# Kernel tuning notes

Measured on AMD Instinct MI355X. Metric: run time of the kernel, lower is better.

The kernel has to match this reference:

```python
import jax, jax.numpy as jnp
import numpy as np

B, L, E, H = 128, 256, 256, 512


def setup_inputs() -> dict:
    key = jax.random.key(0)
    ks = jax.random.split(key, 16)
    s = 0.02
    return {
        "embedded_inputs": jax.random.normal(ks[0], (B, L, E), jnp.float32),
        "decoder_input": jax.random.normal(ks[1], (B, E), jnp.float32),
        "dec_h": jax.random.normal(ks[2], (B, H), jnp.float32),
        "dec_c": jax.random.normal(ks[3], (B, H), jnp.float32),
        "context": jax.random.normal(ks[4], (B, L, H), jnp.float32),
        # Decoder params
        "W_i2h": jax.random.normal(ks[5], (4 * H, E), jnp.float32) * s,
        "b_i2h": jnp.zeros((4 * H,), jnp.float32),
        "W_h2h": jax.random.normal(ks[6], (4 * H, H), jnp.float32) * s,
        "b_h2h": jnp.zeros((4 * H,), jnp.float32),
        "W_out": jax.random.normal(ks[7], (H, 2 * H), jnp.float32) * s,
        "b_out": jnp.zeros((H,), jnp.float32),
        # Attention params
        "W_inp": jax.random.normal(ks[8], (H, H), jnp.float32) * s,
        "b_inp": jnp.zeros((H,), jnp.float32),
        "W_ctx": jax.random.normal(ks[9], (H, H), jnp.float32) * s,  # Conv1d(k=1) kernel squeezed
        "b_ctx": jnp.zeros((H,), jnp.float32),
        "V": jax.random.uniform(ks[10], (H,), jnp.float32, -1.0, 1.0),
    }


def reference(embedded_inputs, decoder_input, dec_h, dec_c, context,
              W_i2h, b_i2h, W_h2h, b_h2h, W_out, b_out,
              W_inp, b_inp, W_ctx, b_ctx, V):
    # Precompute projected context: Conv1d(k=1) == per-position linear. ctx: [B, H, L]
    ctx = jnp.einsum("blh,gh->bgl", context, W_ctx) + b_ctx[None, :, None]
    seq_len = embedded_inputs.shape[1]

    def step(carry, _):
        x, h, c, mask = carry
        gates = x @ W_i2h.T + b_i2h + h @ W_h2h.T + b_h2h
        i, f, g, o = jnp.split(gates, 4, axis=1)
        c_t = jax.nn.sigmoid(f) * c + jax.nn.sigmoid(i) * jnp.tanh(g)
        h_t = jax.nn.sigmoid(o) * jnp.tanh(c_t)
        # attention
        inp = h_t @ W_inp.T + b_inp                              # [B, H]
        scores = jnp.einsum("h,bhl->bl", V, jnp.tanh(inp[:, :, None] + ctx))
        att = jnp.where(mask == 0, -jnp.inf, scores)
        alpha = jax.nn.softmax(att, axis=-1)                     # [B, L]
        hidden = jnp.einsum("bhl,bl->bh", ctx, alpha)
        h_new = jnp.tanh(jnp.concatenate([hidden, h_t], axis=1) @ W_out.T + b_out)
        # pointer selection
        idx = jnp.argmax(alpha * mask, axis=1)                   # [B]
        one_hot = jax.nn.one_hot(idx, seq_len, dtype=mask.dtype)
        mask_new = mask * (1.0 - one_hot)
        next_x = jnp.take_along_axis(embedded_inputs, idx[:, None, None], axis=1)[:, 0, :]
        return (next_x, h_new, c_t, mask_new), (alpha, idx)

    mask0 = jnp.ones((embedded_inputs.shape[0], seq_len), jnp.float32)
    (x_f, h_f, c_f, _), (alphas, ptrs) = jax.lax.scan(
        step, (decoder_input, dec_h, dec_c, mask0), None, length=seq_len)
    outputs = jnp.transpose(alphas, (1, 0, 2))   # [B, L, L]
    pointers = jnp.transpose(ptrs, (1, 0))       # [B, L]
    return outputs, pointers, h_f, c_f
```

## Files before the change

### kernel.cpp

```cpp
#include <hip/hip_runtime.h>

#define B 128
#define L 256
#define E 256
#define H 512
#define NBLK 256
#define NTHR 512

typedef float f4 __attribute__((ext_vector_type(4)));

#define WS_CTX 0u
#define WS_HT  18874368u
#define WS_HH  18939904u
#define WS_HID 19005440u
#define WS_INP 19071232u
#define WS_XT  19136768u
#define WS_FLG 19169536u

#define OUT_ALPHA 0u
#define OUT_PTR   8388608u
#define OUT_H     8421376u
#define OUT_C     8486912u

#define L2E 1.4426950408889634f

__device__ __forceinline__ float fast_rcp(float x) { return __builtin_amdgcn_rcpf(x); }

__device__ __forceinline__ float ftanh(float x) {
  float e = exp2f(x * (2.0f * L2E));
  return 1.0f - 2.0f * fast_rcp(e + 1.0f);
}
__device__ __forceinline__ float fsig(float x) {
  float e = exp2f(-x * L2E);
  return fast_rcp(1.0f + e);
}

#define CLD1(v0, p0)                                                          \
  asm volatile("global_load_dwordx4 %0, %1, off sc0 sc1\n\t"                  \
               "s_waitcnt vmcnt(0)"                                           \
               : "=&v"(v0) : "v"(p0) : "memory")

#define CLD2(va, pa)                                                          \
  asm volatile("global_load_dwordx4 %0, %2, off sc0 sc1\n\t"                  \
               "global_load_dwordx4 %1, %3, off sc0 sc1\n\t"                  \
               "s_waitcnt vmcnt(0)"                                           \
               : "=&v"(va[0]), "=&v"(va[1])                                   \
               : "v"(pa[0]), "v"(pa[1]) : "memory")

#define CLD4(va, pa)                                                          \
  asm volatile("global_load_dwordx4 %0, %4, off sc0 sc1\n\t"                  \
               "global_load_dwordx4 %1, %5, off sc0 sc1\n\t"                  \
               "global_load_dwordx4 %2, %6, off sc0 sc1\n\t"                  \
               "global_load_dwordx4 %3, %7, off sc0 sc1\n\t"                  \
               "s_waitcnt vmcnt(0)"                                           \
               : "=&v"(va[0]), "=&v"(va[1]), "=&v"(va[2]), "=&v"(va[3])       \
               : "v"(pa[0]), "v"(pa[1]), "v"(pa[2]), "v"(pa[3]) : "memory")

#define CLD6(va, pa)                                                          \
  asm volatile("global_load_dwordx4 %0, %6, off sc0 sc1\n\t"                  \
               "global_load_dwordx4 %1, %7, off sc0 sc1\n\t"                  \
               "global_load_dwordx4 %2, %8, off sc0 sc1\n\t"                  \
               "global_load_dwordx4 %3, %9, off sc0 sc1\n\t"                  \
               "global_load_dwordx4 %4, %10, off sc0 sc1\n\t"                 \
               "global_load_dwordx4 %5, %11, off sc0 sc1\n\t"                 \
               "s_waitcnt vmcnt(0)"                                           \
               : "=&v"(va[0]), "=&v"(va[1]), "=&v"(va[2]), "=&v"(va[3]),      \
                 "=&v"(va[4]), "=&v"(va[5])                                   \
               : "v"(pa[0]), "v"(pa[1]), "v"(pa[2]), "v"(pa[3]),              \
                 "v"(pa[4]), "v"(pa[5]) : "memory")

#define CST4_1(p0, v0)                                                        \
  asm volatile("global_store_dwordx4 %0, %1, off sc0 sc1\n\t"                 \
               "s_waitcnt expcnt(0)"                                          \
               :: "v"(p0), "v"(v0) : "memory")

__device__ __forceinline__ void gbar(unsigned* flags, unsigned tgt) {
  asm volatile("s_waitcnt vmcnt(0) lgkmcnt(0) expcnt(0)" ::: "memory");
  __syncthreads();
  if (threadIdx.x == 0) {
    unsigned* p = flags + blockIdx.x * 16;
    asm volatile("global_store_dword %0, %1, off sc0 sc1" :: "v"(p), "v"(tgt) : "memory");
  }
  if (blockIdx.x == 0) {
    if (threadIdx.x < 64) {
      const unsigned* p0 = flags + (threadIdx.x * 4 + 0) * 16;
      const unsigned* p1 = flags + (threadIdx.x * 4 + 1) * 16;
      const unsigned* p2 = flags + (threadIdx.x * 4 + 2) * 16;
      const unsigned* p3 = flags + (threadIdx.x * 4 + 3) * 16;
      for (;;) {
        unsigned f0, f1, f2, f3;
        asm volatile("global_load_dword %0, %4, off sc0 sc1\n\t"
                     "global_load_dword %1, %5, off sc0 sc1\n\t"
                     "global_load_dword %2, %6, off sc0 sc1\n\t"
                     "global_load_dword %3, %7, off sc0 sc1\n\t"
                     "s_waitcnt vmcnt(0)"
                     : "=&v"(f0), "=&v"(f1), "=&v"(f2), "=&v"(f3)
                     : "v"(p0), "v"(p1), "v"(p2), "v"(p3) : "memory");
        if (__all(f0 >= tgt && f1 >= tgt && f2 >= tgt && f3 >= tgt)) break;
        __builtin_amdgcn_s_sleep(1);
      }
    }
    __syncthreads();
    if (threadIdx.x < 8) {
      unsigned* gp = flags + 4096 + threadIdx.x * 16;
      asm volatile("global_store_dword %0, %1, off sc0 sc1" :: "v"(gp), "v"(tgt) : "memory");
    }
  } else {
    if (threadIdx.x == 0) {
      const unsigned* gp = flags + 4096 + (blockIdx.x & 7) * 16;
      for (;;) {
        unsigned g;
        asm volatile("global_load_dword %0, %1, off sc0 sc1\n\ts_waitcnt vmcnt(0)"
                     : "=&v"(g) : "v"(gp) : "memory");
        if (g >= tgt) break;
        __builtin_amdgcn_s_sleep(2);
      }
    }
  }
  __syncthreads();
}

__global__ __launch_bounds__(256) void k_ctx(const float* __restrict__ context,
                                             const float* __restrict__ Wc,
                                             const float* __restrict__ bc,
                                             float* __restrict__ ws) {
  __shared__ float a_lds[64][33];
  __shared__ float b_lds[32][68];
  int t = threadIdx.x;
  int m0 = blockIdx.x * 64;
  int n0 = blockIdx.y * 64;
  int tx = t & 15, ty = t >> 4;
  float acc[4][4] = {};
  for (int kc = 0; kc < 16; ++kc) {
    int k0 = kc * 32;
    __syncthreads();
#pragma unroll
    for (int i = 0; i < 2; ++i) {
      int f40 = t + i * 256;
      int mm = f40 >> 3;
      int k4 = (f40 & 7) * 4;
      float4 v = *(const float4*)&context[(size_t)(m0 + mm) * H + k0 + k4];
      a_lds[mm][k4] = v.x; a_lds[mm][k4 + 1] = v.y; a_lds[mm][k4 + 2] = v.z; a_lds[mm][k4 + 3] = v.w;
    }
#pragma unroll
    for (int i = 0; i < 2; ++i) {
      int f40 = t + i * 256;
      int nn = f40 >> 3;
      int k4 = (f40 & 7) * 4;
      float4 v = *(const float4*)&Wc[(size_t)(n0 + nn) * H + k0 + k4];
      b_lds[k4][nn] = v.x; b_lds[k4 + 1][nn] = v.y; b_lds[k4 + 2][nn] = v.z; b_lds[k4 + 3][nn] = v.w;
    }
    __syncthreads();
#pragma unroll
    for (int kk = 0; kk < 32; ++kk) {
      float4 bv = *(const float4*)&b_lds[kk][tx * 4];
      float a0 = a_lds[ty * 4 + 0][kk], a1 = a_lds[ty * 4 + 1][kk];
      float a2 = a_lds[ty * 4 + 2][kk], a3 = a_lds[ty * 4 + 3][kk];
      acc[0][0] += a0 * bv.x; acc[0][1] += a0 * bv.y; acc[0][2] += a0 * bv.z; acc[0][3] += a0 * bv.w;
      acc[1][0] += a1 * bv.x; acc[1][1] += a1 * bv.y; acc[1][2] += a1 * bv.z; acc[1][3] += a1 * bv.w;
      acc[2][0] += a2 * bv.x; acc[2][1] += a2 * bv.y; acc[2][2] += a2 * bv.z; acc[2][3] += a2 * bv.w;
      acc[3][0] += a3 * bv.x; acc[3][1] += a3 * bv.y; acc[3][2] += a3 * bv.z; acc[3][3] += a3 * bv.w;
    }
  }
  float b0v = bc[n0 + tx * 4], b1v = bc[n0 + tx * 4 + 1], b2v = bc[n0 + tx * 4 + 2], b3v = bc[n0 + tx * 4 + 3];
#pragma unroll
  for (int i = 0; i < 4; ++i) {
    size_t o = WS_CTX + (size_t)(m0 + ty * 4 + i) * H + n0 + tx * 4;
    float4 v; v.x = acc[i][0] + b0v; v.y = acc[i][1] + b1v; v.z = acc[i][2] + b2v; v.w = acc[i][3] + b3v;
    *(float4*)&ws[o] = v;
  }
}

__global__ __launch_bounds__(256) void k_init(const float* __restrict__ dec_h,
                                              const float* __restrict__ dec_in,
                                              float* __restrict__ ws) {
  int flat = blockIdx.x * 256 + threadIdx.x;
  if (flat < 65536) {
    ws[WS_HH + flat] = dec_h[flat];
  } else if (flat < 98304) {
    ws[WS_XT + (flat - 65536)] = dec_in[flat - 65536];
  } else if (flat < 102528) {
    ((unsigned*)(ws + WS_FLG))[flat - 98304] = 0u;
  }
}

__global__ __launch_bounds__(512, 1) void k_main(
    const float* __restrict__ Wi2h, const float* __restrict__ bi2h,
    const float* __restrict__ Wh2h, const float* __restrict__ bh2h,
    const float* __restrict__ Wout, const float* __restrict__ bout,
    const float* __restrict__ Winp, const float* __restrict__ binp,
    const float* __restrict__ Vv,   const float* __restrict__ emb,
    const float* __restrict__ dec_c,
    float* __restrict__ ws,         float* __restrict__ out) {
  __shared__ float s_act[13504];
  __shared__ float s_maskP[256];
  __shared__ float s_mw[8], s_dw[8];
  __shared__ float s_red[4];
  __shared__ int   s_redi[4];
  __shared__ int   s_wc[4], s_wb[4];
  __shared__ int   s_mi, s_cnt;

  unsigned* flags = (unsigned*)(ws + WS_FLG);
  const int bid = blockIdx.x;
  const int t = threadIdx.x;
  const int wv = t >> 6, ln = t & 63;
  unsigned tgt = 0;

  float creg = 0.f;

  if (bid < 128 && t < 256) s_maskP[t] = 1.0f;
  __syncthreads();

  for (int step = 0; step < L; ++step) {
    {
      const int jt = (bid & 7) * 4 + ((bid >> 3) & 3);
      const int bt = bid >> 5;
      const int u0 = jt * 16, b0 = bt * 16;
      float* sact = s_act;
      float* sg   = s_act + 12352;
      f4 va[6]; const float* pa[6]; int sb[6], sq[6];
#pragma unroll
      for (int it = 0; it < 6; ++it) {
        unsigned c = (unsigned)(t + it * 512);
        int bl = (int)(c / 192u);
        int kq = (int)(c - (unsigned)bl * 192u);
        int kg = kq * 4;
        sb[it] = bl; sq[it] = kq;
        pa[it] = (kg < 256) ? ws + WS_XT + (size_t)(b0 + bl) * 256 + kg
                            : ws + WS_HH + (size_t)(b0 + bl) * 512 + (kg - 256);
      }
      CLD6(va, pa);
      __builtin_amdgcn_sched_barrier(0);
#pragma unroll
      for (int it = 0; it < 6; ++it) *(f4*)&sact[sb[it] * 772 + sq[it] * 4] = va[it];
      __syncthreads();

      const int jj = t >> 4, bb = t & 15;
      const int g = jj >> 3, up = (jj & 7) * 2;
      const int r0 = g * 512 + u0 + up;
      float a0 = 0.f, a1 = 0.f;
      {
        const float* w0 = Wi2h + (size_t)r0 * 256;
        const float* w1 = w0 + 256;
        const float* sa = sact + bb * 772;
#pragma unroll 8
        for (int k4 = 0; k4 < 64; ++k4) {
          float4 x = *(const float4*)&sa[k4 * 4];
          float4 p = *(const float4*)&w0[k4 * 4];
          float4 q = *(const float4*)&w1[k4 * 4];
          a0 += p.x * x.x + p.y * x.y + p.z * x.z + p.w * x.w;
          a1 += q.x * x.x + q.y * x.y + q.z * x.z + q.w * x.w;
        }
        const float* v0 = Wh2h + (size_t)r0 * 512;
        const float* v1 = v0 + 512;
        const float* shh = sa + 256;
#pragma unroll 8
        for (int k4 = 0; k4 < 128; ++k4) {
          float4 x = *(const float4*)&shh[k4 * 4];
          float4 p = *(const float4*)&v0[k4 * 4];
          float4 q = *(const float4*)&v1[k4 * 4];
          a0 += p.x * x.x + p.y * x.y + p.z * x.z + p.w * x.w;
          a1 += q.x * x.x + q.y * x.y + q.z * x.z + q.w * x.w;
        }
      }
      sg[(g * 16 + up) * 17 + bb]     = a0;
      sg[(g * 16 + up + 1) * 17 + bb] = a1;
      __syncthreads();
      if (t < 256) {
        const int uu = t >> 4, b2 = t & 15;
        const int j0 = u0 + uu;
        float si_ = sg[(     uu) * 17 + b2] + bi2h[       j0] + bh2h[       j0];
        float sf_ = sg[(16 + uu) * 17 + b2] + bi2h[ 512 + j0] + bh2h[ 512 + j0];
        float sg_ = sg[(32 + uu) * 17 + b2] + bi2h[1024 + j0] + bh2h[1024 + j0];
        float so_ = sg[(48 + uu) * 17 + b2] + bi2h[1536 + j0] + bh2h[1536 + j0];
        if (step == 0) creg = dec_c[(size_t)(b0 + b2) * 512 + j0];
        float cn = fsig(sf_) * creg + fsig(si_) * ftanh(sg_);
        creg = cn;
        float htv = fsig(so_) * ftanh(cn);
        s_act[b2 * 17 + uu] = htv;
        if (step == L - 1) out[OUT_C + (size_t)(b0 + b2) * 512 + j0] = cn;
      }
      __syncthreads();
      if (t < 64) {
        const int b2 = t >> 2, q = t & 3;
        f4 hv;
        hv[0] = s_act[b2 * 17 + q * 4 + 0];
        hv[1] = s_act[b2 * 17 + q * 4 + 1];
        hv[2] = s_act[b2 * 17 + q * 4 + 2];
        hv[3] = s_act[b2 * 17 + q * 4 + 3];
        float* hp = ws + WS_HT + (size_t)(b0 + b2) * 512 + u0 + q * 4;
        CST4_1(hp, hv);
      }
    }
    ++tgt; gbar(flags, tgt);

    {
      const int gt = (bid & 7) * 2 + ((bid >> 3) & 1);
      const int bt = bid >> 4;
      const int g0 = gt * 32, b0 = bt * 8;
      float* si = s_act;
      float* stmp = s_act + 4128;
      f4 va[2]; const float* pa[2];
#pragma unroll
      for (int it = 0; it < 2; ++it) {
        int c = t + it * 512;
        int bl = c >> 7, kq = c & 127;
        pa[it] = ws + WS_HT + (size_t)(b0 + bl) * 512 + kq * 4;
      }
      CLD2(va, pa);
      __builtin_amdgcn_sched_barrier(0);
#pragma unroll
      for (int it = 0; it < 2; ++it) {
        int c = t + it * 512;
        int bl = c >> 7, kq = c & 127;
        *(f4*)&si[bl * 516 + kq * 4] = va[it];
      }
      __syncthreads();
      if (t < 256) {
        const int gl = t >> 3, bb = t & 7;
        const float* w = Winp + (size_t)(g0 + gl) * 512;
        const float* sa = si + bb * 516;
        float acc = 0.f;
#pragma unroll 8
        for (int k4 = 0; k4 < 128; ++k4) {
          float4 ww = *(const float4*)&w[k4 * 4];
          float4 xx = *(const float4*)&sa[k4 * 4];
          acc += ww.x * xx.x + ww.y * xx.y + ww.z * xx.z + ww.w * xx.w;
        }
        stmp[bb * 33 + gl] = acc + binp[g0 + gl];
      }
      __syncthreads();
      if (t < 64) {
        const int bb = t >> 3, q = t & 7;
        f4 v;
        v[0] = stmp[bb * 33 + q * 4 + 0];
        v[1] = stmp[bb * 33 + q * 4 + 1];
        v[2] = stmp[bb * 33 + q * 4 + 2];
        v[3] = stmp[bb * 33 + q * 4 + 3];
        float* p = ws + WS_INP + (size_t)(b0 + bb) * 512 + g0 + q * 4;
        CST4_1(p, v);
      }
    }
    ++tgt; gbar(flags, tgt);

    if (bid < 128) {
      const int b = bid;
      float* s_inp  = s_act;
      float* s_sc   = s_act + 512;
      int*   s_li   = (int*)(s_act + 768);
      float* s_hidp = s_act + 1024;
      float* s_out  = s_act + 5120;
      if (t < 128) {
        f4 v;
        const float* p = ws + WS_INP + (size_t)b * 512 + t * 4;
        CLD1(v, p);
        *(f4*)&s_inp[t * 4] = v;
      }
      __syncthreads();
      const int d0 = ln * 8;
      float inp8[8], v8[8];
#pragma unroll
      for (int i = 0; i < 8; ++i) { inp8[i] = s_inp[d0 + i]; v8[i] = Vv[d0 + i]; }
      bool validl = (t < 256) && (s_maskP[t] != 0.f);
      unsigned long long bal = __ballot(validl);
      if (t < 256 && (t & 63) == 0) s_wc[t >> 6] = (int)__popcll(bal);
      __syncthreads();
      if (t == 0) {
        int base = 0;
#pragma unroll
        for (int i = 0; i < 4; ++i) { s_wb[i] = base; base += s_wc[i]; }
        s_cnt = base;
      }
      __syncthreads();
      if (validl) {
        int idx = s_wb[t >> 6] + (int)__popcll(bal & ((1ull << (t & 63)) - 1ull));
        s_li[idx] = t;
      }
      __syncthreads();
      const int cnt = s_cnt;
      float m = -INFINITY, den = 0.f;
      float hid[8] = {0, 0, 0, 0, 0, 0, 0, 0};
      {
        f4 cur0a, cur0b, cur1a, cur1b, cur2a, cur2b, cur3a, cur3b;
        int l0i, l1i, l2i, l3i;
        int base = wv * 4;
        {
          int s0 = base, s1 = base + 1, s2 = base + 2, s3 = base + 3;
          int a = (s0 < cnt) ? s_li[s0] : 0;  l0i = (s0 < cnt) ? a : -1;
          int bb2 = (s1 < cnt) ? s_li[s1] : 0; l1i = (s1 < cnt) ? bb2 : -1;
          int c = (s2 < cnt) ? s_li[s2] : 0;  l2i = (s2 < cnt) ? c : -1;
          int d = (s3 < cnt) ? s_li[s3] : 0;  l3i = (s3 < cnt) ? d : -1;
          const f4* p0 = (const f4*)(ws + WS_CTX + ((size_t)(b * 256 + a) * 512) + d0);
          const f4* p1 = (const f4*)(ws + WS_CTX + ((size_t)(b * 256 + bb2) * 512) + d0);
          const f4* p2 = (const f4*)(ws + WS_CTX + ((size_t)(b * 256 + c) * 512) + d0);
          const f4* p3 = (const f4*)(ws + WS_CTX + ((size_t)(b * 256 + d) * 512) + d0);
          cur0a = __builtin_nontemporal_load(p0); cur0b = __builtin_nontemporal_load(p0 + 1);
          cur1a = __builtin_nontemporal_load(p1); cur1b = __builtin_nontemporal_load(p1 + 1);
          cur2a = __builtin_nontemporal_load(p2); cur2b = __builtin_nontemporal_load(p2 + 1);
          cur3a = __builtin_nontemporal_load(p3); cur3b = __builtin_nontemporal_load(p3 + 1);
        }
        for (; base < cnt; base += 32) {
          f4 n0a, n0b, n1a, n1b, n2a, n2b, n3a, n3b;
          int nl0, nl1, nl2, nl3;
          {
            int s0 = base + 32, s1 = base + 33, s2 = base + 34, s3 = base + 35;
            int a = (s0 < cnt) ? s_li[s0] : 0;  nl0 = (s0 < cnt) ? a : -1;
            int bb2 = (s1 < cnt) ? s_li[s1] : 0; nl1 = (s1 < cnt) ? bb2 : -1;
            int c = (s2 < cnt) ? s_li[s2] : 0;  nl2 = (s2 < cnt) ? c : -1;
            int d = (s3 < cnt) ? s_li[s3] : 0;  nl3 = (s3 < cnt) ? d : -1;
            const f4* p0 = (const f4*)(ws + WS_CTX + ((size_t)(b * 256 + a) * 512) + d0);
            const f4* p1 = (const f4*)(ws + WS_CTX + ((size_t)(b * 256 + bb2) * 512) + d0);
            const f4* p2 = (const f4*)(ws + WS_CTX + ((size_t)(b * 256 + c) * 512) + d0);
            const f4* p3 = (const f4*)(ws + WS_CTX + ((size_t)(b * 256 + d) * 512) + d0);
            n0a = __builtin_nontemporal_load(p0); n0b = __builtin_nontemporal_load(p0 + 1);
            n1a = __builtin_nontemporal_load(p1); n1b = __builtin_nontemporal_load(p1 + 1);
            n2a = __builtin_nontemporal_load(p2); n2b = __builtin_nontemporal_load(p2 + 1);
            n3a = __builtin_nontemporal_load(p3); n3b = __builtin_nontemporal_load(p3 + 1);
          }
          float sv0, sv1, sv2, sv3;
          {
            float part = v8[0] * ftanh(inp8[0] + cur0a[0]) + v8[1] * ftanh(inp8[1] + cur0a[1])
                       + v8[2] * ftanh(inp8[2] + cur0a[2]) + v8[3] * ftanh(inp8[3] + cur0a[3])
                       + v8[4] * ftanh(inp8[4] + cur0b[0]) + v8[5] * ftanh(inp8[5] + cur0b[1])
                       + v8[6] * ftanh(inp8[6] + cur0b[2]) + v8[7] * ftanh(inp8[7] + cur0b[3]);
#pragma unroll
            for (int off = 32; off > 0; off >>= 1) part += __shfl_xor(part, off);
            if (l0i >= 0 && ln == 0) s_sc[l0i] = part;
            sv0 = (l0i >= 0) ? part : -INFINITY;
          }
          {
            float part = v8[0] * ftanh(inp8[0] + cur1a[0]) + v8[1] * ftanh(inp8[1] + cur1a[1])
                       + v8[2] * ftanh(inp8[2] + cur1a[2]) + v8[3] * ftanh(inp8[3] + cur1a[3])
                       + v8[4] * ftanh(inp8[4] + cur1b[0]) + v8[5] * ftanh(inp8[5] + cur1b[1])
                       + v8[6] * ftanh(inp8[6] + cur1b[2]) + v8[7] * ftanh(inp8[7] + cur1b[3]);
#pragma unroll
            for (int off = 32; off > 0; off >>= 1) part += __shfl_xor(part, off);
            if (l1i >= 0 && ln == 0) s_sc[l1i] = part;
            sv1 = (l1i >= 0) ? part : -INFINITY;
          }
          {
            float part = v8[0] * ftanh(inp8[0] + cur2a[0]) + v8[1] * ftanh(inp8[1] + cur2a[1])
                       + v8[2] * ftanh(inp8[2] + cur2a[2]) + v8[3] * ftanh(inp8[3] + cur2a[3])
                       + v8[4] * ftanh(inp8[4] + cur2b[0]) + v8[5] * ftanh(inp8[5] + cur2b[1])
                       + v8[6] * ftanh(inp8[6] + cur2b[2]) + v8[7] * ftanh(inp8[7] + cur2b[3]);
#pragma unroll
            for (int off = 32; off > 0; off >>= 1) part += __shfl_xor(part, off);
            if (l2i >= 0 && ln == 0) s_sc[l2i] = part;
            sv2 = (l2i >= 0) ? part : -INFINITY;
          }
          {
            float part = v8[0] * ftanh(inp8[0] + cur3a[0]) + v8[1] * ftanh(inp8[1] + cur3a[1])
                       + v8[2] * ftanh(inp8[2] + cur3a[2]) + v8[3] * ftanh(inp8[3] + cur3a[3])
                       + v8[4] * ftanh(inp8[4] + cur3b[0]) + v8[5] * ftanh(inp8[5] + cur3b[1])
                       + v8[6] * ftanh(inp8[6] + cur3b[2]) + v8[7] * ftanh(inp8[7] + cur3b[3]);
#pragma unroll
            for (int off = 32; off > 0; off >>= 1) part += __shfl_xor(part, off);
            if (l3i >= 0 && ln == 0) s_sc[l3i] = part;
            sv3 = (l3i >= 0) ? part : -INFINITY;
          }
          float mn = fmaxf(m, fmaxf(fmaxf(sv0, sv1), fmaxf(sv2, sv3)));
          float scale = exp2f((m - mn) * L2E);
          float e0 = exp2f((sv0 - mn) * L2E);
          float e1 = exp2f((sv1 - mn) * L2E);
          float e2 = exp2f((sv2 - mn) * L2E);
          float e3 = exp2f((sv3 - mn) * L2E);
          den = den * scale + ((e0 + e1) + (e2 + e3));
          hid[0] = hid[0] * scale + e0 * cur0a[0] + e1 * cur1a[0] + e2 * cur2a[0] + e3 * cur3a[0];
          hid[1] = hid[1] * scale + e0 * cur0a[1] + e1 * cur1a[1] + e2 * cur2a[1] + e3 * cur3a[1];
          hid[2] = hid[2] * scale + e0 * cur0a[2] + e1 * cur1a[2] + e2 * cur2a[2] + e3 * cur3a[2];
          hid[3] = hid[3] * scale + e0 * cur0a[3] + e1 * cur1a[3] + e2 * cur2a[3] + e3 * cur3a[3];
          hid[4] = hid[4] * scale + e0 * cur0b[0] + e1 * cur1b[0] + e2 * cur2b[0] + e3 * cur3b[0];
          hid[5] = hid[5] * scale + e0 * cur0b[1] + e1 * cur1b[1] + e2 * cur2b[1] + e3 * cur3b[1];
          hid[6] = hid[6] * scale + e0 * cur0b[2] + e1 * cur1b[2] + e2 * cur2b[2] + e3 * cur3b[2];
          hid[7] = hid[7] * scale + e0 * cur0b[3] + e1 * cur1b[3] + e2 * cur2b[3] + e3 * cur3b[3];
          m = mn;
          cur0a = n0a; cur0b = n0b; cur1a = n1a; cur1b = n1b;
          cur2a = n2a; cur2b = n2b; cur3a = n3a; cur3b = n3b;
          l0i = nl0; l1i = nl1; l2i = nl2; l3i = nl3;
        }
      }
      if (ln == 0) { s_mw[wv] = m; s_dw[wv] = den; }
      __syncthreads();
      float M = s_mw[0];
#pragma unroll
      for (int w = 1; w < 8; ++w) M = fmaxf(M, s_mw[w]);
      float D = 0.f;
#pragma unroll
      for (int w = 0; w < 8; ++w) D += s_dw[w] * exp2f((s_mw[w] - M) * L2E);
      float fac = exp2f((m - M) * L2E);
#pragma unroll
      for (int i = 0; i < 8; ++i) s_hidp[wv * 512 + d0 + i] = hid[i] * fac;
      __syncthreads();
      const float rD = 1.0f / D;
      {
        float hs = 0.f;
#pragma unroll
        for (int w = 0; w < 8; ++w) hs += s_hidp[w * 512 + t];
        s_out[t] = hs * rD;
      }
      float sc = 0.f; bool valid = false;
      if (t < 256) {
        valid = (s_maskP[t] != 0.f);
        sc = s_sc[t];
        float alpha = valid ? exp2f((sc - M) * L2E) * rD : 0.f;
        out[OUT_ALPHA + ((size_t)b * 256 + step) * 256 + t] = alpha;
        float bs = valid ? sc : -INFINITY;
        int bi = t;
#pragma unroll
        for (int off = 32; off > 0; off >>= 1) {
          float os = __shfl_down(bs, off);
          int oi = __shfl_down(bi, off);
          if (os > bs || (os == bs && oi < bi)) { bs = os; bi = oi; }
        }
        if ((t & 63) == 0) { s_red[t >> 6] = bs; s_redi[t >> 6] = bi; }
      }
      __syncthreads();
      if (t == 0) {
        float mm = s_red[0]; int mi = s_redi[0];
#pragma unroll
        for (int w = 1; w < 4; ++w) {
          if (s_red[w] > mm || (s_red[w] == mm && s_redi[w] < mi)) { mm = s_red[w]; mi = s_redi[w]; }
        }
        s_mi = mi;
      }
      __syncthreads();
      const int mi = s_mi;
      if (t < 128) {
        f4 hv = *(const f4*)&s_out[t * 4];
        float* hp = ws + WS_HID + (size_t)b * 512 + t * 4;
        CST4_1(hp, hv);
      }
      if (t < 64) {
        float4 xv = *(const float4*)&emb[((size_t)b * 256 + mi) * 256 + t * 4];
        f4 xq; xq[0] = xv.x; xq[1] = xv.y; xq[2] = xv.z; xq[3] = xv.w;
        float* xp = ws + WS_XT + (size_t)b * 256 + t * 4;
        CST4_1(xp, xq);
      }
      if (t == 0) {
        out[OUT_PTR + (size_t)b * 256 + step] = (float)mi;
        s_maskP[mi] = 0.f;
      }
    }
    ++tgt; gbar(flags, tgt);

    {
      const int rt = (bid & 7) * 2 + ((bid >> 3) & 1);
      const int bt = bid >> 4;
      const int r0 = rt * 32, b0 = bt * 8;
      float* sh = s_act;
      float* stmp = s_act + 8224;
      f4 va[4]; const float* pa[4];
#pragma unroll
      for (int it = 0; it < 4; ++it) {
        int c = t + it * 512;
        int bl = c >> 8, kq = c & 255;
        int kg = kq * 4;
        pa[it] = (kg < 512) ? ws + WS_HID + (size_t)(b0 + bl) * 512 + kg
                            : ws + WS_HT + (size_t)(b0 + bl) * 512 + (kg - 512);
      }
      CLD4(va, pa);
      __builtin_amdgcn_sched_barrier(0);
#pragma unroll
      for (int it = 0; it < 4; ++it) {
        int c = t + it * 512;
        int bl = c >> 8, kq = c & 255;
        *(f4*)&sh[bl * 1028 + kq * 4] = va[it];
      }
      __syncthreads();
      if (t < 256) {
        const int rl = t >> 3, bb = t & 7;
        const float* w = Wout + (size_t)(r0 + rl) * 1024;
        const float* sa = sh + bb * 1028;
        float acc = 0.f;
#pragma unroll 8
        for (int k4 = 0; k4 < 256; ++k4) {
          float4 ww = *(const float4*)&w[k4 * 4];
          float4 xx = *(const float4*)&sa[k4 * 4];
          acc += ww.x * xx.x + ww.y * xx.y + ww.z * xx.z + ww.w * xx.w;
        }
        float h = ftanh(acc + bout[r0 + rl]);
        stmp[bb * 33 + rl] = h;
        if (step == L - 1) out[OUT_H + (size_t)(b0 + bb) * 512 + r0 + rl] = h;
      }
      __syncthreads();
      if (t < 64) {
        const int bb = t >> 3, q = t & 7;
        f4 v;
        v[0] = stmp[bb * 33 + q * 4 + 0];
        v[1] = stmp[bb * 33 + q * 4 + 1];
        v[2] = stmp[bb * 33 + q * 4 + 2];
        v[3] = stmp[bb * 33 + q * 4 + 3];
        float* p = ws + WS_HH + (size_t)(b0 + bb) * 512 + r0 + q * 4;
        CST4_1(p, v);
      }
    }
    ++tgt; gbar(flags, tgt);
  }
}

extern "C" void kernel_launch(void* const* d_in, const int* in_sizes, int n_in,
                              void* d_out, int out_size, void* d_ws, size_t ws_size,
                              hipStream_t stream) {
  (void)in_sizes; (void)n_in; (void)out_size; (void)ws_size;
  const float* emb    = (const float*)d_in[0];
  const float* dec_in = (const float*)d_in[1];
  const float* dec_h  = (const float*)d_in[2];
  const float* dec_c  = (const float*)d_in[3];
  const float* ctx_in = (const float*)d_in[4];
  const float* W_i2h  = (const float*)d_in[5];
  const float* b_i2h  = (const float*)d_in[6];
  const float* W_h2h  = (const float*)d_in[7];
  const float* b_h2h  = (const float*)d_in[8];
  const float* W_out  = (const float*)d_in[9];
  const float* b_out  = (const float*)d_in[10];
  const float* W_inp  = (const float*)d_in[11];
  const float* b_inp  = (const float*)d_in[12];
  const float* W_ctx  = (const float*)d_in[13];
  const float* b_ctx  = (const float*)d_in[14];
  const float* Vv     = (const float*)d_in[15];
  float* out = (float*)d_out;
  float* ws  = (float*)d_ws;

  k_ctx<<<dim3(512, 8), 256, 0, stream>>>(ctx_in, W_ctx, b_ctx, ws);
  k_init<<<401, 256, 0, stream>>>(dec_h, dec_in, ws);
  k_main<<<NBLK, NTHR, 0, stream>>>(W_i2h, b_i2h, W_h2h, b_h2h, W_out, b_out,
                                    W_inp, b_inp, Vv, emb, dec_c, ws, out);
}
```

Before: 16.53 ms.

## Replace global barriers with per-producer flag waits and double-buffered state

```diff
diff --git a/kernel.cpp b/kernel.cpp
--- a/kernel.cpp
+++ b/kernel.cpp
@@ -10,12 +10,17 @@
 typedef float f4 __attribute__((ext_vector_type(4)));
 
 #define WS_CTX 0u
-#define WS_HT  18874368u
-#define WS_HH  18939904u
-#define WS_HID 19005440u
-#define WS_INP 19071232u
-#define WS_XT  19136768u
-#define WS_FLG 19169536u
+#define WS_HT  16777216u
+#define WS_HH  16908288u
+#define WS_HID 17039360u
+#define WS_INP 17170432u
+#define WS_XT  17301504u
+#define WS_FLG 17367040u
+
+#define FLG_PG 0u
+#define FLG_PI 4096u
+#define FLG_PA 8192u
+#define FLG_PH 12288u
 
 #define OUT_ALPHA 0u
 #define OUT_PTR   8388608u
@@ -74,51 +79,28 @@
                "s_waitcnt expcnt(0)"                                          \
                :: "v"(p0), "v"(v0) : "memory")
 
-__device__ __forceinline__ void gbar(unsigned* flags, unsigned tgt) {
-  asm volatile("s_waitcnt vmcnt(0) lgkmcnt(0) expcnt(0)" ::: "memory");
-  __syncthreads();
-  if (threadIdx.x == 0) {
-    unsigned* p = flags + blockIdx.x * 16;
-    asm volatile("global_store_dword %0, %1, off sc0 sc1" :: "v"(p), "v"(tgt) : "memory");
+__device__ __forceinline__ void wait_ge(const unsigned* fp, bool act, unsigned tgt) {
+  for (;;) {
+    unsigned f = tgt;
+    if (act) {
+      asm volatile("global_load_dword %0, %1, off sc0 sc1\n\ts_waitcnt vmcnt(0)"
+                   : "=&v"(f) : "v"(fp) : "memory");
+    }
+    if (__all(f >= tgt)) break;
+    __builtin_amdgcn_s_sleep(1);
   }
-  if (blockIdx.x == 0) {
-    if (threadIdx.x < 64) {
-      const unsigned* p0 = flags + (threadIdx.x * 4 + 0) * 16;
-      const unsigned* p1 = flags + (threadIdx.x * 4 + 1) * 16;
-      const unsigned* p2 = flags + (threadIdx.x * 4 + 2) * 16;
-      const unsigned* p3 = flags + (threadIdx.x * 4 + 3) * 16;
-      for (;;) {
-        unsigned f0, f1, f2, f3;
-        asm volatile("global_load_dword %0, %4, off sc0 sc1\n\t"
-                     "global_load_dword %1, %5, off sc0 sc1\n\t"
-                     "global_load_dword %2, %6, off sc0 sc1\n\t"
-                     "global_load_dword %3, %7, off sc0 sc1\n\t"
-                     "s_waitcnt vmcnt(0)"
-                     : "=&v"(f0), "=&v"(f1), "=&v"(f2), "=&v"(f3)
-                     : "v"(p0), "v"(p1), "v"(p2), "v"(p3) : "memory");
-        if (__all(f0 >= tgt && f1 >= tgt && f2 >= tgt && f3 >= tgt)) break;
-        __builtin_amdgcn_s_sleep(1);
-      }
-    }
-    __syncthreads();
-    if (threadIdx.x < 8) {
-      unsigned* gp = flags + 4096 + threadIdx.x * 16;
-      asm volatile("global_store_dword %0, %1, off sc0 sc1" :: "v"(gp), "v"(tgt) : "memory");
-    }
-  } else {
-    if (threadIdx.x == 0) {
-      const unsigned* gp = flags + 4096 + (blockIdx.x & 7) * 16;
-      for (;;) {
-        unsigned g;
-        asm volatile("global_load_dword %0, %1, off sc0 sc1\n\ts_waitcnt vmcnt(0)"
-                     : "=&v"(g) : "v"(gp) : "memory");
-        if (g >= tgt) break;
-        __builtin_amdgcn_s_sleep(2);
-      }
-    }
-  }
-  __syncthreads();
 }
+
+#define PUBLISH(ARROFF) do {                                                  \
+    asm volatile("s_waitcnt vmcnt(0) lgkmcnt(0) expcnt(0)" ::: "memory");     \
+    __syncthreads();                                                          \
+    if (t == 0) {                                                             \
+      unsigned* fp_ = flags + (ARROFF) + (unsigned)bid * 16u;                 \
+      unsigned v_ = (unsigned)(step + 1);                                     \
+      asm volatile("global_store_dword %0, %1, off sc0 sc1"                   \
+                   :: "v"(fp_), "v"(v_) : "memory");                          \
+    }                                                                         \
+  } while (0)
 
 __global__ __launch_bounds__(256) void k_ctx(const float* __restrict__ context,
                                              const float* __restrict__ Wc,
@@ -179,7 +161,7 @@
     ws[WS_HH + flat] = dec_h[flat];
   } else if (flat < 98304) {
     ws[WS_XT + (flat - 65536)] = dec_in[flat - 65536];
-  } else if (flat < 102528) {
+  } else if (flat < 114688) {
     ((unsigned*)(ws + WS_FLG))[flat - 98304] = 0u;
   }
 }
@@ -204,7 +186,6 @@
   const int bid = blockIdx.x;
   const int t = threadIdx.x;
   const int wv = t >> 6, ln = t & 63;
-  unsigned tgt = 0;
 
   float creg = 0.f;
 
@@ -212,10 +193,29 @@
   __syncthreads();
 
   for (int step = 0; step < L; ++step) {
+    const unsigned pr = (unsigned)(step & 1);
+    float* HTc  = ws + WS_HT  + pr * 65536u;
+    float* HHr  = ws + WS_HH  + pr * 65536u;
+    float* HHw  = ws + WS_HH  + (pr ^ 1u) * 65536u;
+    float* HIDc = ws + WS_HID + pr * 65536u;
+    float* INPc = ws + WS_INP + pr * 65536u;
+    float* XTr  = ws + WS_XT  + pr * 32768u;
+    float* XTw  = ws + WS_XT  + (pr ^ 1u) * 32768u;
+
     {
       const int jt = (bid & 7) * 4 + ((bid >> 3) & 3);
       const int bt = bid >> 5;
       const int u0 = jt * 16, b0 = bt * 16;
+      if (step > 0) {
+        if (wv == 0) {
+          const unsigned* fp = flags;
+          bool act = false;
+          if (ln < 32) { fp = flags + FLG_PH + ((unsigned)bt * 32u + (unsigned)ln) * 16u; act = true; }
+          else if (ln < 48) { fp = flags + FLG_PA + ((unsigned)bt * 16u + (unsigned)(ln - 32)) * 16u; act = true; }
+          wait_ge(fp, act, (unsigned)step);
+        }
+        __syncthreads();
+      }
       float* sact = s_act;
       float* sg   = s_act + 12352;
       f4 va[6]; const float* pa[6]; int sb[6], sq[6];
@@ -226,8 +226,8 @@
         int kq = (int)(c - (unsigned)bl * 192u);
         int kg = kq * 4;
         sb[it] = bl; sq[it] = kq;
-        pa[it] = (kg < 256) ? ws + WS_XT + (size_t)(b0 + bl) * 256 + kg
-                            : ws + WS_HH + (size_t)(b0 + bl) * 512 + (kg - 256);
+        pa[it] = (kg < 256) ? XTr + (size_t)(b0 + bl) * 256 + kg
+                            : HHr + (size_t)(b0 + bl) * 512 + (kg - 256);
       }
       CLD6(va, pa);
       __builtin_amdgcn_sched_barrier(0);
@@ -288,16 +288,20 @@
         hv[1] = s_act[b2 * 17 + q * 4 + 1];
         hv[2] = s_act[b2 * 17 + q * 4 + 2];
         hv[3] = s_act[b2 * 17 + q * 4 + 3];
-        float* hp = ws + WS_HT + (size_t)(b0 + b2) * 512 + u0 + q * 4;
+        float* hp = HTc + (size_t)(b0 + b2) * 512 + u0 + q * 4;
         CST4_1(hp, hv);
       }
-    }
-    ++tgt; gbar(flags, tgt);
+      PUBLISH(FLG_PG);
+    }
 
     {
       const int gt = (bid & 7) * 2 + ((bid >> 3) & 1);
       const int bt = bid >> 4;
       const int g0 = gt * 32, b0 = bt * 8;
+      if (wv == 0)
+        wait_ge(flags + FLG_PG + ((unsigned)(bid >> 5) * 32u + (unsigned)ln) * 16u,
+                ln < 32, (unsigned)(step + 1));
+      __syncthreads();
       float* si = s_act;
       float* stmp = s_act + 4128;
       f4 va[2]; const float* pa[2];
@@ -305,7 +309,7 @@
       for (int it = 0; it < 2; ++it) {
         int c = t + it * 512;
         int bl = c >> 7, kq = c & 127;
-        pa[it] = ws + WS_HT + (size_t)(b0 + bl) * 512 + kq * 4;
+        pa[it] = HTc + (size_t)(b0 + bl) * 512 + kq * 4;
       }
       CLD2(va, pa);
       __builtin_amdgcn_sched_barrier(0);
@@ -337,11 +341,11 @@
         v[1] = stmp[bb * 33 + q * 4 + 1];
         v[2] = stmp[bb * 33 + q * 4 + 2];
         v[3] = stmp[bb * 33 + q * 4 + 3];
-        float* p = ws + WS_INP + (size_t)(b0 + bb) * 512 + g0 + q * 4;
+        float* p = INPc + (size_t)(b0 + bb) * 512 + g0 + q * 4;
         CST4_1(p, v);
       }
-    }
-    ++tgt; gbar(flags, tgt);
+      PUBLISH(FLG_PI);
+    }
 
     if (bid < 128) {
       const int b = bid;
@@ -350,17 +354,6 @@
       int*   s_li   = (int*)(s_act + 768);
       float* s_hidp = s_act + 1024;
       float* s_out  = s_act + 5120;
-      if (t < 128) {
-        f4 v;
-        const float* p = ws + WS_INP + (size_t)b * 512 + t * 4;
-        CLD1(v, p);
-        *(f4*)&s_inp[t * 4] = v;
-      }
-      __syncthreads();
-      const int d0 = ln * 8;
-      float inp8[8], v8[8];
-#pragma unroll
-      for (int i = 0; i < 8; ++i) { inp8[i] = s_inp[d0 + i]; v8[i] = Vv[d0 + i]; }
       bool validl = (t < 256) && (s_maskP[t] != 0.f);
       unsigned long long bal = __ballot(validl);
       if (t < 256 && (t & 63) == 0) s_wc[t >> 6] = (int)__popcll(bal);
@@ -378,106 +371,119 @@
       }
       __syncthreads();
       const int cnt = s_cnt;
+      const int d0 = ln * 8;
+      f4 cur0a, cur0b, cur1a, cur1b, cur2a, cur2b, cur3a, cur3b;
+      int l0i, l1i, l2i, l3i;
+      const int base0 = wv * 4;
+      {
+        int s0 = base0, s1 = base0 + 1, s2 = base0 + 2, s3 = base0 + 3;
+        int a = (s0 < cnt) ? s_li[s0] : 0;  l0i = (s0 < cnt) ? a : -1;
+        int bb2 = (s1 < cnt) ? s_li[s1] : 0; l1i = (s1 < cnt) ? bb2 : -1;
+        int c = (s2 < cnt) ? s_li[s2] : 0;  l2i = (s2 < cnt) ? c : -1;
+        int d = (s3 < cnt) ? s_li[s3] : 0;  l3i = (s3 < cnt) ? d : -1;
+        const f4* p0 = (const f4*)(ws + WS_CTX + ((size_t)(b * 256 + a) * 512) + d0);
+        const f4* p1 = (const f4*)(ws + WS_CTX + ((size_t)(b * 256 + bb2) * 512) + d0);
+        const f4* p2 = (const f4*)(ws + WS_CTX + ((size_t)(b * 256 + c) * 512) + d0);
+        const f4* p3 = (const f4*)(ws + WS_CTX + ((size_t)(b * 256 + d) * 512) + d0);
+        cur0a = __builtin_nontemporal_load(p0); cur0b = __builtin_nontemporal_load(p0 + 1);
+        cur1a = __builtin_nontemporal_load(p1); cur1b = __builtin_nontemporal_load(p1 + 1);
+        cur2a = __builtin_nontemporal_load(p2); cur2b = __builtin_nontemporal_load(p2 + 1);
+        cur3a = __builtin_nontemporal_load(p3); cur3b = __builtin_nontemporal_load(p3 + 1);
+      }
+      if (wv == 0)
+        wait_ge(flags + FLG_PI + ((unsigned)(b >> 3) * 16u + (unsigned)ln) * 16u,
+                ln < 16, (unsigned)(step + 1));
+      __syncthreads();
+      if (t < 128) {
+        f4 v;
+        const float* p = INPc + (size_t)b * 512 + t * 4;
+        CLD1(v, p);
+        *(f4*)&s_inp[t * 4] = v;
+      }
+      __syncthreads();
+      float inp8[8], v8[8];
+#pragma unroll
+      for (int i = 0; i < 8; ++i) { inp8[i] = s_inp[d0 + i]; v8[i] = Vv[d0 + i]; }
       float m = -INFINITY, den = 0.f;
       float hid[8] = {0, 0, 0, 0, 0, 0, 0, 0};
-      {
-        f4 cur0a, cur0b, cur1a, cur1b, cur2a, cur2b, cur3a, cur3b;
-        int l0i, l1i, l2i, l3i;
-        int base = wv * 4;
+      for (int base = base0; base < cnt; base += 32) {
+        f4 n0a, n0b, n1a, n1b, n2a, n2b, n3a, n3b;
+        int nl0, nl1, nl2, nl3;
         {
-          int s0 = base, s1 = base + 1, s2 = base + 2, s3 = base + 3;
-          int a = (s0 < cnt) ? s_li[s0] : 0;  l0i = (s0 < cnt) ? a : -1;
-          int bb2 = (s1 < cnt) ? s_li[s1] : 0; l1i = (s1 < cnt) ? bb2 : -1;
-          int c = (s2 < cnt) ? s_li[s2] : 0;  l2i = (s2 < cnt) ? c : -1;
-          int d = (s3 < cnt) ? s_li[s3] : 0;  l3i = (s3 < cnt) ? d : -1;
+          int s0 = base + 32, s1 = base + 33, s2 = base + 34, s3 = base + 35;
+          int a = (s0 < cnt) ? s_li[s0] : 0;  nl0 = (s0 < cnt) ? a : -1;
+          int bb2 = (s1 < cnt) ? s_li[s1] : 0; nl1 = (s1 < cnt) ? bb2 : -1;
+          int c = (s2 < cnt) ? s_li[s2] : 0;  nl2 = (s2 < cnt) ? c : -1;
+          int d = (s3 < cnt) ? s_li[s3] : 0;  nl3 = (s3 < cnt) ? d : -1;
           const f4* p0 = (const f4*)(ws + WS_CTX + ((size_t)(b * 256 + a) * 512) + d0);
           const f4* p1 = (const f4*)(ws + WS_CTX + ((size_t)(b * 256 + bb2) * 512) + d0);
           const f4* p2 = (const f4*)(ws + WS_CTX + ((size_t)(b * 256 + c) * 512) + d0);
           const f4* p3 = (const f4*)(ws + WS_CTX + ((size_t)(b * 256 + d) * 512) + d0);
-          cur0a = __builtin_nontemporal_load(p0); cur0b = __builtin_nontemporal_load(p0 + 1);
-          cur1a = __builtin_nontemporal_load(p1); cur1b = __builtin_nontemporal_load(p1 + 1);
-          cur2a = __builtin_nontemporal_load(p2); cur2b = __builtin_nontemporal_load(p2 + 1);
-          cur3a = __builtin_nontemporal_load(p3); cur3b = __builtin_nontemporal_load(p3 + 1);
-        }
-        for (; base < cnt; base += 32) {
-          f4 n0a, n0b, n1a, n1b, n2a, n2b, n3a, n3b;
-          int nl0, nl1, nl2, nl3;
-          {
-            int s0 = base + 32, s1 = base + 33, s2 = base + 34, s3 = base + 35;
-            int a = (s0 < cnt) ? s_li[s0] : 0;  nl0 = (s0 < cnt) ? a : -1;
-            int bb2 = (s1 < cnt) ? s_li[s1] : 0; nl1 = (s1 < cnt) ? bb2 : -1;
-            int c = (s2 < cnt) ? s_li[s2] : 0;  nl2 = (s2 < cnt) ? c : -1;
-            int d = (s3 < cnt) ? s_li[s3] : 0;  nl3 = (s3 < cnt) ? d : -1;
-            const f4* p0 = (const f4*)(ws + WS_CTX + ((size_t)(b * 256 + a) * 512) + d0);
-            const f4* p1 = (const f4*)(ws + WS_CTX + ((size_t)(b * 256 + bb2) * 512) + d0);
-            const f4* p2 = (const f4*)(ws + WS_CTX + ((size_t)(b * 256 + c) * 512) + d0);
-            const f4* p3 = (const f4*)(ws + WS_CTX + ((size_t)(b * 256 + d) * 512) + d0);
-            n0a = __builtin_nontemporal_load(p0); n0b = __builtin_nontemporal_load(p0 + 1);
-            n1a = __builtin_nontemporal_load(p1); n1b = __builtin_nontemporal_load(p1 + 1);
-            n2a = __builtin_nontemporal_load(p2); n2b = __builtin_nontemporal_load(p2 + 1);
-            n3a = __builtin_nontemporal_load(p3); n3b = __builtin_nontemporal_load(p3 + 1);
-          }
-          float sv0, sv1, sv2, sv3;
-          {
-            float part = v8[0] * ftanh(inp8[0] + cur0a[0]) + v8[1] * ftanh(inp8[1] + cur0a[1])
-                       + v8[2] * ftanh(inp8[2] + cur0a[2]) + v8[3] * ftanh(inp8[3] + cur0a[3])
-                       + v8[4] * ftanh(inp8[4] + cur0b[0]) + v8[5] * ftanh(inp8[5] + cur0b[1])
-                       + v8[6] * ftanh(inp8[6] + cur0b[2]) + v8[7] * ftanh(inp8[7] + cur0b[3]);
-#pragma unroll
-            for (int off = 32; off > 0; off >>= 1) part += __shfl_xor(part, off);
-            if (l0i >= 0 && ln == 0) s_sc[l0i] = part;
-            sv0 = (l0i >= 0) ? part : -INFINITY;
-          }
-          {
-            float part = v8[0] * ftanh(inp8[0] + cur1a[0]) + v8[1] * ftanh(inp8[1] + cur1a[1])
-                       + v8[2] * ftanh(inp8[2] + cur1a[2]) + v8[3] * ftanh(inp8[3] + cur1a[3])
-                       + v8[4] * ftanh(inp8[4] + cur1b[0]) + v8[5] * ftanh(inp8[5] + cur1b[1])
-                       + v8[6] * ftanh(inp8[6] + cur1b[2]) + v8[7] * ftanh(inp8[7] + cur1b[3]);
-#pragma unroll
-            for (int off = 32; off > 0; off >>= 1) part += __shfl_xor(part, off);
-            if (l1i >= 0 && ln == 0) s_sc[l1i] = part;
-            sv1 = (l1i >= 0) ? part : -INFINITY;
-          }
-          {
-            float part = v8[0] * ftanh(inp8[0] + cur2a[0]) + v8[1] * ftanh(inp8[1] + cur2a[1])
-                       + v8[2] * ftanh(inp8[2] + cur2a[2]) + v8[3] * ftanh(inp8[3] + cur2a[3])
-                       + v8[4] * ftanh(inp8[4] + cur2b[0]) + v8[5] * ftanh(inp8[5] + cur2b[1])
-                       + v8[6] * ftanh(inp8[6] + cur2b[2]) + v8[7] * ftanh(inp8[7] + cur2b[3]);
-#pragma unroll
-            for (int off = 32; off > 0; off >>= 1) part += __shfl_xor(part, off);
-            if (l2i >= 0 && ln == 0) s_sc[l2i] = part;
-            sv2 = (l2i >= 0) ? part : -INFINITY;
-          }
-          {
-            float part = v8[0] * ftanh(inp8[0] + cur3a[0]) + v8[1] * ftanh(inp8[1] + cur3a[1])
-                       + v8[2] * ftanh(inp8[2] + cur3a[2]) + v8[3] * ftanh(inp8[3] + cur3a[3])
-                       + v8[4] * ftanh(inp8[4] + cur3b[0]) + v8[5] * ftanh(inp8[5] + cur3b[1])
-                       + v8[6] * ftanh(inp8[6] + cur3b[2]) + v8[7] * ftanh(inp8[7] + cur3b[3]);
-#pragma unroll
-            for (int off = 32; off > 0; off >>= 1) part += __shfl_xor(part, off);
-            if (l3i >= 0 && ln == 0) s_sc[l3i] = part;
-            sv3 = (l3i >= 0) ? part : -INFINITY;
-          }
-          float mn = fmaxf(m, fmaxf(fmaxf(sv0, sv1), fmaxf(sv2, sv3)));
-          float scale = exp2f((m - mn) * L2E);
-          float e0 = exp2f((sv0 - mn) * L2E);
-          float e1 = exp2f((sv1 - mn) * L2E);
-          float e2 = exp2f((sv2 - mn) * L2E);
-          float e3 = exp2f((sv3 - mn) * L2E);
-          den = den * scale + ((e0 + e1) + (e2 + e3));
-          hid[0] = hid[0] * scale + e0 * cur0a[0] + e1 * cur1a[0] + e2 * cur2a[0] + e3 * cur3a[0];
-          hid[1] = hid[1] * scale + e0 * cur0a[1] + e1 * cur1a[1] + e2 * cur2a[1] + e3 * cur3a[1];
-          hid[2] = hid[2] * scale + e0 * cur0a[2] + e1 * cur1a[2] + e2 * cur2a[2] + e3 * cur3a[2];
-          hid[3] = hid[3] * scale + e0 * cur0a[3] + e1 * cur1a[3] + e2 * cur2a[3] + e3 * cur3a[3];
-          hid[4] = hid[4] * scale + e0 * cur0b[0] + e1 * cur1b[0] + e2 * cur2b[0] + e3 * cur3b[0];
-          hid[5] = hid[5] * scale + e0 * cur0b[1] + e1 * cur1b[1] + e2 * cur2b[1] + e3 * cur3b[1];
-          hid[6] = hid[6] * scale + e0 * cur0b[2] + e1 * cur1b[2] + e2 * cur2b[2] + e3 * cur3b[2];
-          hid[7] = hid[7] * scale + e0 * cur0b[3] + e1 * cur1b[3] + e2 * cur2b[3] + e3 * cur3b[3];
-          m = mn;
-          cur0a = n0a; cur0b = n0b; cur1a = n1a; cur1b = n1b;
-          cur2a = n2a; cur2b = n2b; cur3a = n3a; cur3b = n3b;
-          l0i = nl0; l1i = nl1; l2i = nl2; l3i = nl3;
-        }
+          n0a = __builtin_nontemporal_load(p0); n0b = __builtin_nontemporal_load(p0 + 1);
+          n1a = __builtin_nontemporal_load(p1); n1b = __builtin_nontemporal_load(p1 + 1);
+          n2a = __builtin_nontemporal_load(p2); n2b = __builtin_nontemporal_load(p2 + 1);
+          n3a = __builtin_nontemporal_load(p3); n3b = __builtin_nontemporal_load(p3 + 1);
+        }
+        float sv0, sv1, sv2, sv3;
+        {
+          float part = v8[0] * ftanh(inp8[0] + cur0a[0]) + v8[1] * ftanh(inp8[1] + cur0a[1])
+                     + v8[2] * ftanh(inp8[2] + cur0a[2]) + v8[3] * ftanh(inp8[3] + cur0a[3])
+                     + v8[4] * ftanh(inp8[4] + cur0b[0]) + v8[5] * ftanh(inp8[5] + cur0b[1])
+                     + v8[6] * ftanh(inp8[6] + cur0b[2]) + v8[7] * ftanh(inp8[7] + cur0b[3]);
+#pragma unroll
+          for (int off = 32; off > 0; off >>= 1) part += __shfl_xor(part, off);
+          if (l0i >= 0 && ln == 0) s_sc[l0i] = part;
+          sv0 = (l0i >= 0) ? part : -INFINITY;
+        }
+        {
+          float part = v8[0] * ftanh(inp8[0] + cur1a[0]) + v8[1] * ftanh(inp8[1] + cur1a[1])
+                     + v8[2] * ftanh(inp8[2] + cur1a[2]) + v8[3] * ftanh(inp8[3] + cur1a[3])
+                     + v8[4] * ftanh(inp8[4] + cur1b[0]) + v8[5] * ftanh(inp8[5] + cur1b[1])
+                     + v8[6] * ftanh(inp8[6] + cur1b[2]) + v8[7] * ftanh(inp8[7] + cur1b[3]);
+#pragma unroll
+          for (int off = 32; off > 0; off >>= 1) part += __shfl_xor(part, off);
+          if (l1i >= 0 && ln == 0) s_sc[l1i] = part;
+          sv1 = (l1i >= 0) ? part : -INFINITY;
+        }
+        {
+          float part = v8[0] * ftanh(inp8[0] + cur2a[0]) + v8[1] * ftanh(inp8[1] + cur2a[1])
+                     + v8[2] * ftanh(inp8[2] + cur2a[2]) + v8[3] * ftanh(inp8[3] + cur2a[3])
+                     + v8[4] * ftanh(inp8[4] + cur2b[0]) + v8[5] * ftanh(inp8[5] + cur2b[1])
+                     + v8[6] * ftanh(inp8[6] + cur2b[2]) + v8[7] * ftanh(inp8[7] + cur2b[3]);
+#pragma unroll
+          for (int off = 32; off > 0; off >>= 1) part += __shfl_xor(part, off);
+          if (l2i >= 0 && ln == 0) s_sc[l2i] = part;
+          sv2 = (l2i >= 0) ? part : -INFINITY;
+        }
+        {
+          float part = v8[0] * ftanh(inp8[0] + cur3a[0]) + v8[1] * ftanh(inp8[1] + cur3a[1])
+                     + v8[2] * ftanh(inp8[2] + cur3a[2]) + v8[3] * ftanh(inp8[3] + cur3a[3])
+                     + v8[4] * ftanh(inp8[4] + cur3b[0]) + v8[5] * ftanh(inp8[5] + cur3b[1])
+                     + v8[6] * ftanh(inp8[6] + cur3b[2]) + v8[7] * ftanh(inp8[7] + cur3b[3]);
+#pragma unroll
+          for (int off = 32; off > 0; off >>= 1) part += __shfl_xor(part, off);
+          if (l3i >= 0 && ln == 0) s_sc[l3i] = part;
+          sv3 = (l3i >= 0) ? part : -INFINITY;
+        }
+        float mn = fmaxf(m, fmaxf(fmaxf(sv0, sv1), fmaxf(sv2, sv3)));
+        float scale = exp2f((m - mn) * L2E);
+        float e0 = exp2f((sv0 - mn) * L2E);
+        float e1 = exp2f((sv1 - mn) * L2E);
+        float e2 = exp2f((sv2 - mn) * L2E);
+        float e3 = exp2f((sv3 - mn) * L2E);
+        den = den * scale + ((e0 + e1) + (e2 + e3));
+        hid[0] = hid[0] * scale + e0 * cur0a[0] + e1 * cur1a[0] + e2 * cur2a[0] + e3 * cur3a[0];
+        hid[1] = hid[1] * scale + e0 * cur0a[1] + e1 * cur1a[1] + e2 * cur2a[1] + e3 * cur3a[1];
+        hid[2] = hid[2] * scale + e0 * cur0a[2] + e1 * cur1a[2] + e2 * cur2a[2] + e3 * cur3a[2];
+        hid[3] = hid[3] * scale + e0 * cur0a[3] + e1 * cur1a[3] + e2 * cur2a[3] + e3 * cur3a[3];
+        hid[4] = hid[4] * scale + e0 * cur0b[0] + e1 * cur1b[0] + e2 * cur2b[0] + e3 * cur3b[0];
+        hid[5] = hid[5] * scale + e0 * cur0b[1] + e1 * cur1b[1] + e2 * cur2b[1] + e3 * cur3b[1];
+        hid[6] = hid[6] * scale + e0 * cur0b[2] + e1 * cur1b[2] + e2 * cur2b[2] + e3 * cur3b[2];
+        hid[7] = hid[7] * scale + e0 * cur0b[3] + e1 * cur1b[3] + e2 * cur2b[3] + e3 * cur3b[3];
+        m = mn;
+        cur0a = n0a; cur0b = n0b; cur1a = n1a; cur1b = n1b;
+        cur2a = n2a; cur2b = n2b; cur3a = n3a; cur3b = n3b;
+        l0i = nl0; l1i = nl1; l2i = nl2; l3i = nl3;
       }
       if (ln == 0) { s_mw[wv] = m; s_dw[wv] = den; }
       __syncthreads();
@@ -527,21 +533,21 @@
       const int mi = s_mi;
       if (t < 128) {
         f4 hv = *(const f4*)&s_out[t * 4];
-        float* hp = ws + WS_HID + (size_t)b * 512 + t * 4;
+        float* hp = HIDc + (size_t)b * 512 + t * 4;
         CST4_1(hp, hv);
       }
       if (t < 64) {
         float4 xv = *(const float4*)&emb[((size_t)b * 256 + mi) * 256 + t * 4];
         f4 xq; xq[0] = xv.x; xq[1] = xv.y; xq[2] = xv.z; xq[3] = xv.w;
-        float* xp = ws + WS_XT + (size_t)b * 256 + t * 4;
+        float* xp = XTw + (size_t)b * 256 + t * 4;
         CST4_1(xp, xq);
       }
       if (t == 0) {
         out[OUT_PTR + (size_t)b * 256 + step] = (float)mi;
         s_maskP[mi] = 0.f;
       }
-    }
-    ++tgt; gbar(flags, tgt);
+      PUBLISH(FLG_PA);
+    }
 
     {
       const int rt = (bid & 7) * 2 + ((bid >> 3) & 1);
@@ -555,16 +561,37 @@
         int c = t + it * 512;
         int bl = c >> 8, kq = c & 255;
         int kg = kq * 4;
-        pa[it] = (kg < 512) ? ws + WS_HID + (size_t)(b0 + bl) * 512 + kg
-                            : ws + WS_HT + (size_t)(b0 + bl) * 512 + (kg - 512);
-      }
-      CLD4(va, pa);
-      __builtin_amdgcn_sched_barrier(0);
-#pragma unroll
-      for (int it = 0; it < 4; ++it) {
-        int c = t + it * 512;
-        int bl = c >> 8, kq = c & 255;
-        *(f4*)&sh[bl * 1028 + kq * 4] = va[it];
+        pa[it] = (kg < 512) ? HIDc + (size_t)(b0 + bl) * 512 + kg
+                            : HTc + (size_t)(b0 + bl) * 512 + (kg - 512);
+      }
+      const bool isHT = (t & 128);
+      if (wv == 0)
+        wait_ge(flags + FLG_PG + ((unsigned)(bid >> 5) * 32u + (unsigned)ln) * 16u,
+                ln < 32, (unsigned)(step + 1));
+      __syncthreads();
+      if (isHT) {
+        CLD4(va, pa);
+        __builtin_amdgcn_sched_barrier(0);
+#pragma unroll
+        for (int it = 0; it < 4; ++it) {
+          int c = t + it * 512;
+          int bl = c >> 8, kq = c & 255;
+          *(f4*)&sh[bl * 1028 + kq * 4] = va[it];
+        }
+      }
+      if (wv == 0)
+        wait_ge(flags + FLG_PA + ((unsigned)b0 + (unsigned)ln) * 16u,
+                ln < 8, (unsigned)(step + 1));
+      __syncthreads();
+      if (!isHT) {
+        CLD4(va, pa);
+        __builtin_amdgcn_sched_barrier(0);
+#pragma unroll
+        for (int it = 0; it < 4; ++it) {
+          int c = t + it * 512;
+          int bl = c >> 8, kq = c & 255;
+          *(f4*)&sh[bl * 1028 + kq * 4] = va[it];
+        }
       }
       __syncthreads();
       if (t < 256) {
@@ -590,11 +617,11 @@
         v[1] = stmp[bb * 33 + q * 4 + 1];
         v[2] = stmp[bb * 33 + q * 4 + 2];
         v[3] = stmp[bb * 33 + q * 4 + 3];
-        float* p = ws + WS_HH + (size_t)(b0 + bb) * 512 + r0 + q * 4;
+        float* p = HHw + (size_t)(b0 + bb) * 512 + r0 + q * 4;
         CST4_1(p, v);
       }
-    }
-    ++tgt; gbar(flags, tgt);
+      PUBLISH(FLG_PH);
+    }
   }
 }
 
@@ -622,7 +649,7 @@
   float* ws  = (float*)d_ws;
 
   k_ctx<<<dim3(512, 8), 256, 0, stream>>>(ctx_in, W_ctx, b_ctx, ws);
-  k_init<<<401, 256, 0, stream>>>(dec_h, dec_in, ws);
+  k_init<<<448, 256, 0, stream>>>(dec_h, dec_in, ws);
   k_main<<<NBLK, NTHR, 0, stream>>>(W_i2h, b_i2h, W_h2h, b_h2h, W_out, b_out,
                                     W_inp, b_inp, Vv, emb, dec_c, ws, out);
 }
```

Result: slower. 17.17 ms (+3.9%).
